# Optimization experiments

Measured on AMD Instinct MI355X. Metric: run time of the kernel, lower is better.

The kernel has to match this reference:

```python
import jax, jax.numpy as jnp
import numpy as np

NB_STEPS = 50
ALPHA = 0.9
NUM_RNN_STEPS = 2
B = 4096
NUM_FEATURE = 100
IN_D = 5
HIDDEN = [64, 64, 64]
P1 = (1.1, 1.1, 1.5, 2.0, 2.5)   # IntegrandNN_outer_level powers
P2 = (1.5, 2.0, 2.5, 3.0, 3.5)   # IntegrandNN powers


def _cc(nb_steps):
    # Clenshaw-Curtis weights/steps, identical to UMNN's compute_cc_weights
    n = nb_steps
    i = np.arange(n + 1, dtype=np.float64).reshape(-1, 1)
    lam = np.cos(i @ i.T * np.pi / n)
    lam[:, 0] = 0.5
    lam[:, -1] *= 0.5
    lam = lam * 2.0 / n
    W = np.zeros(n + 1)
    even = np.arange(0, n + 1, 2)
    W[even] = 2.0 / (1.0 - even.astype(np.float64) ** 2)
    W[0] = 1.0
    ccw = (lam.T @ W).astype(np.float32)                         # [n+1]
    steps = np.cos(np.arange(n + 1) * np.pi / n).astype(np.float32)  # [n+1]
    return jnp.asarray(ccw), jnp.asarray(steps)

CC_W, CC_S = _cc(NB_STEPS)


def _mlp(xh, Ws, bs):
    # Linear+ReLU stack with ELU on the last layer (ReLU popped, ELU appended)
    h = xh
    for W, b in zip(Ws[:-1], bs[:-1]):
        h = jax.nn.relu(h @ W.T + b)
    return jax.nn.elu(h @ Ws[-1].T + bs[-1])


def _integrand(x, h, Ws, bs, Wf, powers):
    z = _mlp(jnp.concatenate([x, h], axis=1), Ws, bs) + 1.0      # [N,1], z >= 0
    feats = jnp.concatenate([z ** p for p in powers], axis=1)    # [N,5]
    return jax.nn.relu((1.0 / (feats + 1.0)) @ Wf.T)             # [N,1]


def _integrate(x0, xT, h, f):
    # ParallelNeuralIntegral forward: CC quadrature of f from x0 to xT
    Bn, S = x0.shape[0], NB_STEPS + 1
    X = x0[:, None, :] + (xT - x0)[:, None, :] * (CC_S[None, :, None] + 1.0) / 2.0  # [B,S,1]
    hs = jnp.broadcast_to(h[:, None, :], (Bn, S, h.shape[1])).reshape(-1, h.shape[1])
    dz = f(X.reshape(-1, 1), hs).reshape(Bn, S, 1)
    return (dz * CC_W[None, :, None]).sum(1) * (xT - x0) / 2.0   # [B,1]


def setup_inputs() -> dict:
    key = jax.random.key(0)
    ks = jax.random.split(key, 24)
    def lin(k, o, i):
        return jax.random.normal(k, (o, i), jnp.float32) / np.sqrt(i)
    d = {}
    d["x_"] = jax.random.normal(ks[0], (B, NUM_FEATURE), jnp.float32)
    d["h_"] = jax.random.normal(ks[1], (B, IN_D - 1), jnp.float32)
    d["log_weight"] = jnp.ones((1, NUM_FEATURE), jnp.float32)     # reset_parameters -> 1
    d["sigmoid_param"] = jnp.zeros((1,), jnp.float32)
    sizes = [IN_D] + HIDDEN + [1]
    for tag, base in (("f1", 2), ("f2", 12)):
        for li, (i, o) in enumerate(zip(sizes[:-1], sizes[1:])):
            d[f"{tag}_W{li}"] = lin(ks[base + 2 * li], o, i)
            d[f"{tag}_b{li}"] = jnp.zeros((o,), jnp.float32)
        d[f"{tag}_Wf"] = jnp.abs(lin(ks[base + 9], 1, 5))         # reset_params -> abs
    return d


def reference(x_, h_, log_weight, sigmoid_param,
              f1_W0, f1_b0, f1_W1, f1_b1, f1_W2, f1_b2, f1_W3, f1_b3, f1_Wf,
              f2_W0, f2_b0, f2_W1, f2_b1, f2_W2, f2_b2, f2_W3, f2_b3, f2_Wf):
    f1Ws = [f1_W0, f1_W1, f1_W2, f1_W3]; f1bs = [f1_b0, f1_b1, f1_b2, f1_b3]
    f2Ws = [f2_W0, f2_W1, f2_W2, f2_W3]; f2bs = [f2_b0, f2_b1, f2_b2, f2_b3]
    f1 = lambda x, h: _integrand(x, h, f1Ws, f1bs, f1_Wf, P1)
    f2 = lambda x, h: _integrand(x, h, f2Ws, f2bs, f2_Wf, P2)

    # modular function: linear to [B,1] then sum over dim 1 -> [B,1]
    xm = jnp.sum(x_ * log_weight[0], axis=1, keepdims=True)
    lam = jax.nn.sigmoid(sigmoid_param[0])

    I1 = jnp.zeros_like(xm)
    I2 = jnp.zeros_like(xm)
    out_first = None
    for _ in range(NUM_RNN_STEPS):
        x = (1.0 - lam) * xm + lam * I1
        x2 = (1.0 - lam) * xm + lam * I2
        out_first = f1(x2, h_)
        I1 = _integrate(jnp.zeros_like(x), x, h_, f1)
        xmax = jnp.max(x2) + 10.0
        xfinal = jnp.zeros_like(x) + xmax
        I2 = (1.0 / ALPHA) * _integrate(x2, xfinal, h_, f2)
    return I1, out_first, I2
```

## Files before the change

### kernel.cpp

```cpp
#include <hip/hip_runtime.h>
#include <math.h>

typedef _Float16 half8v __attribute__((ext_vector_type(8)));
typedef _Float16 half4v __attribute__((ext_vector_type(4)));
typedef _Float16 half2v __attribute__((ext_vector_type(2)));
typedef float float4v __attribute__((ext_vector_type(4)));

#define BB    4096
#define NS    51
#define INV_ALPHA (1.0f/0.9f)

#define WS_CCW   0
#define WS_CCS   64
#define WS_LAM   128
#define WS_KEY64 160
#define WS_PM    256
#define WS_XM    512
#define WS_X     (WS_XM + BB)
#define WS_X2    (WS_X + BB)
#define WS_H     16384
#define H_NET    8192
#define H_W2     4096
#define H_W0     16384
#define H_W3     20480

#if defined(__has_builtin)
#if __has_builtin(__builtin_amdgcn_rcpf)
#define FRCP(x) __builtin_amdgcn_rcpf(x)
#endif
#if __has_builtin(__builtin_amdgcn_exp2f)
#define FEXP2(x) __builtin_amdgcn_exp2f(x)
#endif
#if __has_builtin(__builtin_amdgcn_logf)
#define FLOG2(x) __builtin_amdgcn_logf(x)
#endif
#endif
#ifndef FRCP
#define FRCP(x) (1.0f / (x))
#endif
#ifndef FEXP2
#define FEXP2(x) exp2f(x)
#endif
#ifndef FLOG2
#define FLOG2(x) log2f(x)
#endif

__device__ __forceinline__ unsigned fkey(float f) {
    int i = __float_as_int(f);
    return (i >= 0) ? ((unsigned)i + 0x80000000u) : ~(unsigned)i;
}
__device__ __forceinline__ float fkey_inv(unsigned k) {
    return (k & 0x80000000u) ? __int_as_float((int)(k - 0x80000000u))
                             : __int_as_float((int)~k);
}

__device__ __forceinline__ int swz(int row, int cb) {
    return (row << 6) + (((cb ^ (row & 7)) & 7) << 3);
}

__device__ __forceinline__ half4v pk_relu4(float4v c) {
#if defined(__has_builtin) && __has_builtin(__builtin_amdgcn_cvt_pkrtz)
    half2v a = __builtin_bit_cast(half2v,
        __builtin_amdgcn_cvt_pkrtz(fmaxf(c[0], 0.0f), fmaxf(c[1], 0.0f)));
    half2v b = __builtin_bit_cast(half2v,
        __builtin_amdgcn_cvt_pkrtz(fmaxf(c[2], 0.0f), fmaxf(c[3], 0.0f)));
    half4v o; o[0] = a[0]; o[1] = a[1]; o[2] = b[0]; o[3] = b[1];
    return o;
#else
    half4v o;
    o[0] = (_Float16)fmaxf(c[0], 0.0f); o[1] = (_Float16)fmaxf(c[1], 0.0f);
    o[2] = (_Float16)fmaxf(c[2], 0.0f); o[3] = (_Float16)fmaxf(c[3], 0.0f);
    return o;
#endif
}

__global__ void k_setup(const float* __restrict__ x_, const float* __restrict__ lw,
                        const float* __restrict__ sp,
                        const float* __restrict__ f1W0, const float* __restrict__ f1W1,
                        const float* __restrict__ f1W2, const float* __restrict__ f1W3,
                        const float* __restrict__ f2W0, const float* __restrict__ f2W1,
                        const float* __restrict__ f2W2, const float* __restrict__ f2W3,
                        float* __restrict__ ws) {
    _Float16* wh = (_Float16*)(ws + WS_H);
    const int blk = blockIdx.x, tid = threadIdx.x;
    if (blk < 256) {
        int wave = tid >> 6, lane = tid & 63;
        float vmax = -1e30f;
        for (int r = 0; r < 4; ++r) {
            int row = blk * 16 + wave * 4 + r;
            float v = 0.0f;
            for (int i = lane; i < 100; i += 64) v = fmaf(x_[row * 100 + i], lw[i], v);
            #pragma unroll
            for (int off = 32; off > 0; off >>= 1) v += __shfl_xor(v, off, 64);
            if (lane == 0) ws[WS_XM + row] = v;
            vmax = fmaxf(vmax, v);
        }
        __shared__ float sm[4];
        if (lane == 0) sm[wave] = vmax;
        __syncthreads();
        if (tid == 0)
            ws[WS_PM + blk] = fmaxf(fmaxf(sm[0], sm[1]), fmaxf(sm[2], sm[3]));
    } else if (blk < 272) {
        int t = (blk - 256) * 256 + tid;
        wh[t]                = (_Float16)f1W1[t];
        wh[H_W2 + t]         = (_Float16)f1W2[t];
        wh[H_NET + t]        = (_Float16)f2W1[t];
        wh[H_NET + H_W2 + t] = (_Float16)f2W2[t];
        if (t < 2048) {
            int j = t >> 5, k = t & 31;
            wh[H_W0 + t]        = (k < 5) ? (_Float16)f1W0[j * 5 + k] : (_Float16)0.0f;
            wh[H_W0 + 2048 + t] = (k < 5) ? (_Float16)f2W0[j * 5 + k] : (_Float16)0.0f;
        }
        if (t < 64) {
            wh[H_W3 + t]      = (_Float16)f1W3[t];
            wh[H_W3 + 64 + t] = (_Float16)f2W3[t];
        }
    } else {
        if (tid < 64) ((unsigned*)ws)[WS_KEY64 + tid] = 0u;
        if (tid == 64) ws[WS_LAM] = 1.0f / (1.0f + expf(-sp[0]));
        if (tid >= 128 && tid <= 178) {
            int s = tid - 128;
            ws[WS_CCS + s] = cospif((float)s / 50.0f);
            float acc = 0.0f;
            for (int a = 0; a <= 50; ++a) {
                float w;
                if (a == 0) w = 1.0f;
                else if ((a & 1) == 0) w = 2.0f / (1.0f - (float)(a * a));
                else continue;
                float l;
                if (s == 0) l = 0.5f;
                else {
                    int m = (a * s) % 100;
                    l = cospif((float)m / 50.0f);
                    if (s == 50) l *= 0.5f;
                }
                acc += l * 0.04f * w;
            }
            ws[WS_CCW + s] = acc;
        }
    }
}

__global__ __launch_bounds__(64, 4) void k_int(
    int mode, float* __restrict__ ws, const float* __restrict__ h_,
    const float* __restrict__ f1b0, const float* __restrict__ f1b1,
    const float* __restrict__ f1b2, const float* __restrict__ f1b3,
    const float* __restrict__ f1Wf,
    const float* __restrict__ f2b0, const float* __restrict__ f2b1,
    const float* __restrict__ f2b2, const float* __restrict__ f2b3,
    const float* __restrict__ f2Wf,
    float* __restrict__ out)
{
    __shared__ _Float16 act[64 * 64];

    const int blk = blockIdx.x;
    const int lane = threadIdx.x;
    const int lo = lane & 15, q = lane >> 4;

    const float* xm = ws + WS_XM;
    const float* xarr = ws + WS_X;
    const float* x2arr = ws + WS_X2;
    const _Float16* wh = (const _Float16*)(ws + WS_H);
    const float lam = ws[WS_LAM];
    const float oml = 1.0f - lam;

    int kind, b = 0, b0 = 0;
    if (blk < 4096)      { kind = 0; b = blk; }
    else if (blk < 8192) { kind = 1; b = blk - 4096; }
    else                 { kind = 2; b0 = (blk - 8192) * 64; b = b0 + lane; }

    float xmax = 0.0f, xb = 0.0f, x0 = 0.0f;
    float4 h4u = {0, 0, 0, 0};
    if (kind == 0) {
        xb = mode ? xarr[b] : oml * xm[b];
        h4u = ((const float4*)h_)[b];
    } else if (kind == 1) {
        if (mode) {
            float v = fkey_inv(((const unsigned*)ws)[WS_KEY64 + lane]);
            #pragma unroll
            for (int off = 32; off > 0; off >>= 1) v = fmaxf(v, __shfl_xor(v, off, 64));
            xmax = v + 10.0f;
        } else {
            const float* pm = ws + WS_PM;
            float v = fmaxf(fmaxf(pm[lane], pm[lane + 64]),
                            fmaxf(pm[lane + 128], pm[lane + 192]));
            #pragma unroll
            for (int off = 32; off > 0; off >>= 1) v = fmaxf(v, __shfl_xor(v, off, 64));
            xmax = oml * v + 10.0f;
        }
        x0 = mode ? x2arr[b] : oml * xm[b];
        h4u = ((const float4*)h_)[b];
    }

    const bool u2 = (kind == 1);
    const _Float16* W0h = wh + H_W0 + (u2 ? 2048 : 0);
    const _Float16* W1h = wh + (u2 ? H_NET : 0);
    const _Float16* W2h = W1h + H_W2;
    const _Float16* W3h = wh + H_W3 + (u2 ? 64 : 0);
    const float* B0 = u2 ? f2b0 : f1b0;
    const float* B1 = u2 ? f2b1 : f1b1;
    const float* B2 = u2 ? f2b2 : f1b2;
    const float* B3 = u2 ? f2b3 : f1b3;
    const float* WF = u2 ? f2Wf : f1Wf;
    const float p0 = u2 ? 1.5f : 1.1f;
    const float p1 = u2 ? 2.0f : 1.1f;
    const float p2 = u2 ? 2.5f : 1.5f;
    const float p3 = u2 ? 3.0f : 2.0f;
    const float p4 = u2 ? 3.5f : 2.5f;

    {
        half8v Bf0[4];
        #pragma unroll
        for (int n = 0; n < 4; ++n) {
            int r = 16 * n + lo;
            float xr; float4 hr;
            if (kind == 2) {
                int idx = b0 + r;
                xr = x2arr[idx];
                hr = ((const float4*)h_)[idx];
            } else {
                int si = r > 50 ? 50 : r;
                float t = (ws[WS_CCS + si] + 1.0f) * 0.5f;
                xr = (kind == 0) ? xb * t : x0 + (xmax - x0) * t;
                hr = h4u;
            }
            half8v e;
            e[0] = (_Float16)xr; e[1] = (_Float16)hr.x; e[2] = (_Float16)hr.y;
            e[3] = (_Float16)hr.z; e[4] = (_Float16)hr.w;
            e[5] = (_Float16)0.0f; e[6] = (_Float16)0.0f; e[7] = (_Float16)0.0f;
            half8v z;
            #pragma unroll
            for (int t2 = 0; t2 < 8; ++t2) z[t2] = (_Float16)0.0f;
            Bf0[n] = (q == 0) ? e : z;
        }
        #pragma unroll
        for (int m = 0; m < 4; ++m) {
            half8v Af = *(const half8v*)(W0h + (16 * m + lo) * 32 + q * 8);
            float4v bb = *(const float4v*)(B0 + 16 * m + q * 4);
            #pragma unroll
            for (int n = 0; n < 4; ++n) {
                float4v c = __builtin_amdgcn_mfma_f32_16x16x32_f16(Af, Bf0[n], bb, 0, 0, 0);
                *(half4v*)(act + swz(16 * n + lo, 2 * m + (q >> 1)) + 4 * (q & 1)) = pk_relu4(c);
            }
        }
    }

    {
        half8v Bf[2][4];
        #pragma unroll
        for (int kb = 0; kb < 2; ++kb)
            #pragma unroll
            for (int n = 0; n < 4; ++n)
                Bf[kb][n] = *(const half8v*)(act + swz(16 * n + lo, 4 * kb + q));
        #pragma unroll
        for (int m = 0; m < 4; ++m) {
            half8v A0 = *(const half8v*)(W1h + (16 * m + lo) * 64 + q * 8);
            half8v A1 = *(const half8v*)(W1h + (16 * m + lo) * 64 + 32 + q * 8);
            float4v bb = *(const float4v*)(B1 + 16 * m + q * 4);
            #pragma unroll
            for (int n = 0; n < 4; ++n) {
                float4v c = __builtin_amdgcn_mfma_f32_16x16x32_f16(A0, Bf[0][n], bb, 0, 0, 0);
                c = __builtin_amdgcn_mfma_f32_16x16x32_f16(A1, Bf[1][n], c, 0, 0, 0);
                *(half4v*)(act + swz(16 * n + lo, 2 * m + (q >> 1)) + 4 * (q & 1)) = pk_relu4(c);
            }
        }
    }

    float part[4] = {0.0f, 0.0f, 0.0f, 0.0f};
    {
        half8v Bf[2][4];
        #pragma unroll
        for (int kb = 0; kb < 2; ++kb)
            #pragma unroll
            for (int n = 0; n < 4; ++n)
                Bf[kb][n] = *(const half8v*)(act + swz(16 * n + lo, 4 * kb + q));
        #pragma unroll
        for (int m = 0; m < 4; ++m) {
            half8v A0 = *(const half8v*)(W2h + (16 * m + lo) * 64 + q * 8);
            half8v A1 = *(const half8v*)(W2h + (16 * m + lo) * 64 + 32 + q * 8);
            float4v bb = *(const float4v*)(B2 + 16 * m + q * 4);
            half4v w3 = *(const half4v*)(W3h + 16 * m + 4 * q);
            #pragma unroll
            for (int n = 0; n < 4; ++n) {
                float4v c = __builtin_amdgcn_mfma_f32_16x16x32_f16(A0, Bf[0][n], bb, 0, 0, 0);
                c = __builtin_amdgcn_mfma_f32_16x16x32_f16(A1, Bf[1][n], c, 0, 0, 0);
                #pragma unroll
                for (int e = 0; e < 4; ++e)
                    part[n] = fmaf((float)w3[e], fmaxf(c[e], 0.0f), part[n]);
            }
        }
    }

    #pragma unroll
    for (int n = 0; n < 4; ++n) {
        part[n] += __shfl_xor(part[n], 16, 64);
        part[n] += __shfl_xor(part[n], 32, 64);
    }
    float y = B3[0] + (q == 0 ? part[0] : q == 1 ? part[1] : q == 2 ? part[2] : part[3]);

    if (y <= 0.0f) y = FEXP2(y * 1.44269504f) - 1.0f;
    float z = y + 1.0f;
    float lg = FLOG2(z);
    float g = WF[0] * FRCP(FEXP2(p0 * lg) + 1.0f)
            + WF[1] * FRCP(FEXP2(p1 * lg) + 1.0f)
            + WF[2] * FRCP(FEXP2(p2 * lg) + 1.0f)
            + WF[3] * FRCP(FEXP2(p3 * lg) + 1.0f)
            + WF[4] * FRCP(FEXP2(p4 * lg) + 1.0f);
    float val = fmaxf(g, 0.0f);

    if (kind == 2) { out[BB + b] = val; return; }

    float c = (lane <= 50) ? ws[WS_CCW + lane] * val : 0.0f;
    #pragma unroll
    for (int off = 32; off > 0; off >>= 1) c += __shfl_xor(c, off, 64);

    if (lane == 0) {
        if (kind == 0) {
            float I1 = c * xb * 0.5f;
            out[b] = I1;
            if (!mode) ws[WS_X + b] = oml * xm[b] + lam * I1;
        } else {
            float I2 = c * (xmax - x0) * 0.5f * INV_ALPHA;
            out[2 * BB + b] = I2;
            if (!mode) {
                float x2n = oml * xm[b] + lam * I2;
                ws[WS_X2 + b] = x2n;
                atomicMax((unsigned*)ws + WS_KEY64 + (b & 63), fkey(x2n));
            }
        }
    }
}

extern "C" void kernel_launch(void* const* d_in, const int* in_sizes, int n_in,
                              void* d_out, int out_size, void* d_ws, size_t ws_size,
                              hipStream_t stream) {
    const float* x_  = (const float*)d_in[0];
    const float* h_  = (const float*)d_in[1];
    const float* lw  = (const float*)d_in[2];
    const float* sp  = (const float*)d_in[3];
    const float* f1W0 = (const float*)d_in[4];   const float* f1b0 = (const float*)d_in[5];
    const float* f1W1 = (const float*)d_in[6];   const float* f1b1 = (const float*)d_in[7];
    const float* f1W2 = (const float*)d_in[8];   const float* f1b2 = (const float*)d_in[9];
    const float* f1W3 = (const float*)d_in[10];  const float* f1b3 = (const float*)d_in[11];
    const float* f1Wf = (const float*)d_in[12];
    const float* f2W0 = (const float*)d_in[13];  const float* f2b0 = (const float*)d_in[14];
    const float* f2W1 = (const float*)d_in[15];  const float* f2b1 = (const float*)d_in[16];
    const float* f2W2 = (const float*)d_in[17];  const float* f2b2 = (const float*)d_in[18];
    const float* f2W3 = (const float*)d_in[19];  const float* f2b3 = (const float*)d_in[20];
    const float* f2Wf = (const float*)d_in[21];
    float* out = (float*)d_out;
    float* ws  = (float*)d_ws;

    k_setup<<<273, 256, 0, stream>>>(x_, lw, sp,
                                     f1W0, f1W1, f1W2, f1W3,
                                     f2W0, f2W1, f2W2, f2W3, ws);
    k_int<<<8192, 64, 0, stream>>>(0, ws, h_,
        f1b0, f1b1, f1b2, f1b3, f1Wf, f2b0, f2b1, f2b2, f2b3, f2Wf, out);
    k_int<<<8256, 64, 0, stream>>>(1, ws, h_,
        f1b0, f1b1, f1b2, f1b3, f1Wf, f2b0, f2b1, f2b2, f2b3, f2Wf, out);
}
```

Baseline: 158.2 us.

## Make integrand kernel persistent and keep MLP weights in registers across items

The integration kernel now launches 2048 blocks, and each loops over four batch items (plus one out_first tile for 64 blocks in mode 1). The weights, biases, quadrature steps and weights are loaded into registers once per block instead of once per item. Launch bounds drop from 4 to 2 waves per EU to make room for the extra registers. This cuts repeated weight loads and block launch overhead, but lowers occupancy and leaves the out_first tiles as a tail on 64 blocks.

Result: faster. 144.9 us (-8.4%).

```diff
diff --git a/kernel.cpp b/kernel.cpp
--- a/kernel.cpp
+++ b/kernel.cpp
@@ -141,7 +141,7 @@
     }
 }
 
-__global__ __launch_bounds__(64, 4) void k_int(
+__global__ __launch_bounds__(64, 2) void k_int(
     int mode, float* __restrict__ ws, const float* __restrict__ h_,
     const float* __restrict__ f1b0, const float* __restrict__ f1b1,
     const float* __restrict__ f1b2, const float* __restrict__ f1b3,
@@ -164,35 +164,9 @@
     const float lam = ws[WS_LAM];
     const float oml = 1.0f - lam;
 
-    int kind, b = 0, b0 = 0;
-    if (blk < 4096)      { kind = 0; b = blk; }
-    else if (blk < 8192) { kind = 1; b = blk - 4096; }
-    else                 { kind = 2; b0 = (blk - 8192) * 64; b = b0 + lane; }
-
-    float xmax = 0.0f, xb = 0.0f, x0 = 0.0f;
-    float4 h4u = {0, 0, 0, 0};
-    if (kind == 0) {
-        xb = mode ? xarr[b] : oml * xm[b];
-        h4u = ((const float4*)h_)[b];
-    } else if (kind == 1) {
-        if (mode) {
-            float v = fkey_inv(((const unsigned*)ws)[WS_KEY64 + lane]);
-            #pragma unroll
-            for (int off = 32; off > 0; off >>= 1) v = fmaxf(v, __shfl_xor(v, off, 64));
-            xmax = v + 10.0f;
-        } else {
-            const float* pm = ws + WS_PM;
-            float v = fmaxf(fmaxf(pm[lane], pm[lane + 64]),
-                            fmaxf(pm[lane + 128], pm[lane + 192]));
-            #pragma unroll
-            for (int off = 32; off > 0; off >>= 1) v = fmaxf(v, __shfl_xor(v, off, 64));
-            xmax = oml * v + 10.0f;
-        }
-        x0 = mode ? x2arr[b] : oml * xm[b];
-        h4u = ((const float4*)h_)[b];
-    }
-
-    const bool u2 = (kind == 1);
+    const bool u2 = (blk >= 1024);
+    const int kb0 = u2 ? blk - 1024 : blk;
+
     const _Float16* W0h = wh + H_W0 + (u2 ? 2048 : 0);
     const _Float16* W1h = wh + (u2 ? H_NET : 0);
     const _Float16* W2h = W1h + H_W2;
@@ -208,124 +182,177 @@
     const float p3 = u2 ? 3.0f : 2.0f;
     const float p4 = u2 ? 3.5f : 2.5f;
 
-    {
+    half8v A0w[4], A1w[4][2], A2w[4][2];
+    float4v b0r[4], b1r[4], b2r[4];
+    half4v w3r[4];
+    #pragma unroll
+    for (int m = 0; m < 4; ++m) {
+        A0w[m]    = *(const half8v*)(W0h + (16 * m + lo) * 32 + q * 8);
+        A1w[m][0] = *(const half8v*)(W1h + (16 * m + lo) * 64 + q * 8);
+        A1w[m][1] = *(const half8v*)(W1h + (16 * m + lo) * 64 + 32 + q * 8);
+        A2w[m][0] = *(const half8v*)(W2h + (16 * m + lo) * 64 + q * 8);
+        A2w[m][1] = *(const half8v*)(W2h + (16 * m + lo) * 64 + 32 + q * 8);
+        b0r[m] = *(const float4v*)(B0 + 16 * m + q * 4);
+        b1r[m] = *(const float4v*)(B1 + 16 * m + q * 4);
+        b2r[m] = *(const float4v*)(B2 + 16 * m + q * 4);
+        w3r[m] = *(const half4v*)(W3h + 16 * m + 4 * q);
+    }
+    const float B3s = B3[0];
+    const float wf0 = WF[0], wf1 = WF[1], wf2 = WF[2], wf3 = WF[3], wf4 = WF[4];
+
+    float t_r[4];
+    #pragma unroll
+    for (int n = 0; n < 4; ++n) {
+        int r = 16 * n + lo;
+        t_r[n] = (ws[WS_CCS + (r > 50 ? 50 : r)] + 1.0f) * 0.5f;
+    }
+    const float ccw_l = (lane <= 50) ? ws[WS_CCW + lane] : 0.0f;
+
+    float xmax = 0.0f;
+    if (u2) {
+        if (mode) {
+            float v = fkey_inv(((const unsigned*)ws)[WS_KEY64 + lane]);
+            #pragma unroll
+            for (int off = 32; off > 0; off >>= 1) v = fmaxf(v, __shfl_xor(v, off, 64));
+            xmax = v + 10.0f;
+        } else {
+            const float* pm = ws + WS_PM;
+            float v = fmaxf(fmaxf(pm[lane], pm[lane + 64]),
+                            fmaxf(pm[lane + 128], pm[lane + 192]));
+            #pragma unroll
+            for (int off = 32; off > 0; off >>= 1) v = fmaxf(v, __shfl_xor(v, off, 64));
+            xmax = oml * v + 10.0f;
+        }
+    }
+
+    const int nitems = (mode && !u2 && blk < 64) ? 5 : 4;
+
+    #pragma clang loop unroll(disable)
+    for (int it = 0; it < nitems; ++it) {
+        const bool last = (it == 4);
+        int b = kb0 + 1024 * it;
+        float xb = 0.0f, x0 = 0.0f;
+        float4 h4u = {0, 0, 0, 0};
+
         half8v Bf0[4];
+        if (last) {
+            int b0i = blk * 64;
+            #pragma unroll
+            for (int n = 0; n < 4; ++n) {
+                int idx = b0i + 16 * n + lo;
+                float xr = x2arr[idx];
+                float4 hr = ((const float4*)h_)[idx];
+                half8v e;
+                e[0] = (_Float16)xr; e[1] = (_Float16)hr.x; e[2] = (_Float16)hr.y;
+                e[3] = (_Float16)hr.z; e[4] = (_Float16)hr.w;
+                e[5] = (_Float16)0.0f; e[6] = (_Float16)0.0f; e[7] = (_Float16)0.0f;
+                half8v z;
+                #pragma unroll
+                for (int t2 = 0; t2 < 8; ++t2) z[t2] = (_Float16)0.0f;
+                Bf0[n] = (q == 0) ? e : z;
+            }
+        } else {
+            if (!u2) xb = mode ? xarr[b] : oml * xm[b];
+            else     x0 = mode ? x2arr[b] : oml * xm[b];
+            h4u = ((const float4*)h_)[b];
+            #pragma unroll
+            for (int n = 0; n < 4; ++n) {
+                float xr = (!u2) ? xb * t_r[n] : x0 + (xmax - x0) * t_r[n];
+                half8v e;
+                e[0] = (_Float16)xr; e[1] = (_Float16)h4u.x; e[2] = (_Float16)h4u.y;
+                e[3] = (_Float16)h4u.z; e[4] = (_Float16)h4u.w;
+                e[5] = (_Float16)0.0f; e[6] = (_Float16)0.0f; e[7] = (_Float16)0.0f;
+                half8v z;
+                #pragma unroll
+                for (int t2 = 0; t2 < 8; ++t2) z[t2] = (_Float16)0.0f;
+                Bf0[n] = (q == 0) ? e : z;
+            }
+        }
+
+        #pragma unroll
+        for (int m = 0; m < 4; ++m)
+            #pragma unroll
+            for (int n = 0; n < 4; ++n) {
+                float4v c = __builtin_amdgcn_mfma_f32_16x16x32_f16(A0w[m], Bf0[n], b0r[m], 0, 0, 0);
+                *(half4v*)(act + swz(16 * n + lo, 2 * m + (q >> 1)) + 4 * (q & 1)) = pk_relu4(c);
+            }
+
+        {
+            half8v Bf[2][4];
+            #pragma unroll
+            for (int kb = 0; kb < 2; ++kb)
+                #pragma unroll
+                for (int n = 0; n < 4; ++n)
+                    Bf[kb][n] = *(const half8v*)(act + swz(16 * n + lo, 4 * kb + q));
+            #pragma unroll
+            for (int m = 0; m < 4; ++m)
+                #pragma unroll
+                for (int n = 0; n < 4; ++n) {
+                    float4v c = __builtin_amdgcn_mfma_f32_16x16x32_f16(A1w[m][0], Bf[0][n], b1r[m], 0, 0, 0);
+                    c = __builtin_amdgcn_mfma_f32_16x16x32_f16(A1w[m][1], Bf[1][n], c, 0, 0, 0);
+                    *(half4v*)(act + swz(16 * n + lo, 2 * m + (q >> 1)) + 4 * (q & 1)) = pk_relu4(c);
+                }
+        }
+
+        float part[4] = {0.0f, 0.0f, 0.0f, 0.0f};
+        {
+            half8v Bf[2][4];
+            #pragma unroll
+            for (int kb = 0; kb < 2; ++kb)
+                #pragma unroll
+                for (int n = 0; n < 4; ++n)
+                    Bf[kb][n] = *(const half8v*)(act + swz(16 * n + lo, 4 * kb + q));
+            #pragma unroll
+            for (int m = 0; m < 4; ++m)
+                #pragma unroll
+                for (int n = 0; n < 4; ++n) {
+                    float4v c = __builtin_amdgcn_mfma_f32_16x16x32_f16(A2w[m][0], Bf[0][n], b2r[m], 0, 0, 0);
+                    c = __builtin_amdgcn_mfma_f32_16x16x32_f16(A2w[m][1], Bf[1][n], c, 0, 0, 0);
+                    #pragma unroll
+                    for (int e = 0; e < 4; ++e)
+                        part[n] = fmaf((float)w3r[m][e], fmaxf(c[e], 0.0f), part[n]);
+                }
+        }
+
         #pragma unroll
         for (int n = 0; n < 4; ++n) {
-            int r = 16 * n + lo;
-            float xr; float4 hr;
-            if (kind == 2) {
-                int idx = b0 + r;
-                xr = x2arr[idx];
-                hr = ((const float4*)h_)[idx];
+            part[n] += __shfl_xor(part[n], 16, 64);
+            part[n] += __shfl_xor(part[n], 32, 64);
+        }
+        float y = B3s + (q == 0 ? part[0] : q == 1 ? part[1] : q == 2 ? part[2] : part[3]);
+
+        if (y <= 0.0f) y = FEXP2(y * 1.44269504f) - 1.0f;
+        float z = y + 1.0f;
+        float lg = FLOG2(z);
+        float g = wf0 * FRCP(FEXP2(p0 * lg) + 1.0f)
+                + wf1 * FRCP(FEXP2(p1 * lg) + 1.0f)
+                + wf2 * FRCP(FEXP2(p2 * lg) + 1.0f)
+                + wf3 * FRCP(FEXP2(p3 * lg) + 1.0f)
+                + wf4 * FRCP(FEXP2(p4 * lg) + 1.0f);
+        float val = fmaxf(g, 0.0f);
+
+        if (last) {
+            out[BB + blk * 64 + lane] = val;
+            continue;
+        }
+
+        float c = ccw_l * val;
+        #pragma unroll
+        for (int off = 32; off > 0; off >>= 1) c += __shfl_xor(c, off, 64);
+
+        if (lane == 0) {
+            if (!u2) {
+                float I1 = c * xb * 0.5f;
+                out[b] = I1;
+                if (!mode) ws[WS_X + b] = oml * xm[b] + lam * I1;
             } else {
-                int si = r > 50 ? 50 : r;
-                float t = (ws[WS_CCS + si] + 1.0f) * 0.5f;
-                xr = (kind == 0) ? xb * t : x0 + (xmax - x0) * t;
-                hr = h4u;
-            }
-            half8v e;
-            e[0] = (_Float16)xr; e[1] = (_Float16)hr.x; e[2] = (_Float16)hr.y;
-            e[3] = (_Float16)hr.z; e[4] = (_Float16)hr.w;
-            e[5] = (_Float16)0.0f; e[6] = (_Float16)0.0f; e[7] = (_Float16)0.0f;
-            half8v z;
-            #pragma unroll
-            for (int t2 = 0; t2 < 8; ++t2) z[t2] = (_Float16)0.0f;
-            Bf0[n] = (q == 0) ? e : z;
-        }
-        #pragma unroll
-        for (int m = 0; m < 4; ++m) {
-            half8v Af = *(const half8v*)(W0h + (16 * m + lo) * 32 + q * 8);
-            float4v bb = *(const float4v*)(B0 + 16 * m + q * 4);
-            #pragma unroll
-            for (int n = 0; n < 4; ++n) {
-                float4v c = __builtin_amdgcn_mfma_f32_16x16x32_f16(Af, Bf0[n], bb, 0, 0, 0);
-                *(half4v*)(act + swz(16 * n + lo, 2 * m + (q >> 1)) + 4 * (q & 1)) = pk_relu4(c);
-            }
-        }
-    }
-
-    {
-        half8v Bf[2][4];
-        #pragma unroll
-        for (int kb = 0; kb < 2; ++kb)
-            #pragma unroll
-            for (int n = 0; n < 4; ++n)
-                Bf[kb][n] = *(const half8v*)(act + swz(16 * n + lo, 4 * kb + q));
-        #pragma unroll
-        for (int m = 0; m < 4; ++m) {
-            half8v A0 = *(const half8v*)(W1h + (16 * m + lo) * 64 + q * 8);
-            half8v A1 = *(const half8v*)(W1h + (16 * m + lo) * 64 + 32 + q * 8);
-            float4v bb = *(const float4v*)(B1 + 16 * m + q * 4);
-            #pragma unroll
-            for (int n = 0; n < 4; ++n) {
-                float4v c = __builtin_amdgcn_mfma_f32_16x16x32_f16(A0, Bf[0][n], bb, 0, 0, 0);
-                c = __builtin_amdgcn_mfma_f32_16x16x32_f16(A1, Bf[1][n], c, 0, 0, 0);
-                *(half4v*)(act + swz(16 * n + lo, 2 * m + (q >> 1)) + 4 * (q & 1)) = pk_relu4(c);
-            }
-        }
-    }
-
-    float part[4] = {0.0f, 0.0f, 0.0f, 0.0f};
-    {
-        half8v Bf[2][4];
-        #pragma unroll
-        for (int kb = 0; kb < 2; ++kb)
-            #pragma unroll
-            for (int n = 0; n < 4; ++n)
-                Bf[kb][n] = *(const half8v*)(act + swz(16 * n + lo, 4 * kb + q));
-        #pragma unroll
-        for (int m = 0; m < 4; ++m) {
-            half8v A0 = *(const half8v*)(W2h + (16 * m + lo) * 64 + q * 8);
-            half8v A1 = *(const half8v*)(W2h + (16 * m + lo) * 64 + 32 + q * 8);
-            float4v bb = *(const float4v*)(B2 + 16 * m + q * 4);
-            half4v w3 = *(const half4v*)(W3h + 16 * m + 4 * q);
-            #pragma unroll
-            for (int n = 0; n < 4; ++n) {
-                float4v c = __builtin_amdgcn_mfma_f32_16x16x32_f16(A0, Bf[0][n], bb, 0, 0, 0);
-                c = __builtin_amdgcn_mfma_f32_16x16x32_f16(A1, Bf[1][n], c, 0, 0, 0);
-                #pragma unroll
-                for (int e = 0; e < 4; ++e)
-                    part[n] = fmaf((float)w3[e], fmaxf(c[e], 0.0f), part[n]);
-            }
-        }
-    }
-
-    #pragma unroll
-    for (int n = 0; n < 4; ++n) {
-        part[n] += __shfl_xor(part[n], 16, 64);
-        part[n] += __shfl_xor(part[n], 32, 64);
-    }
-    float y = B3[0] + (q == 0 ? part[0] : q == 1 ? part[1] : q == 2 ? part[2] : part[3]);
-
-    if (y <= 0.0f) y = FEXP2(y * 1.44269504f) - 1.0f;
-    float z = y + 1.0f;
-    float lg = FLOG2(z);
-    float g = WF[0] * FRCP(FEXP2(p0 * lg) + 1.0f)
-            + WF[1] * FRCP(FEXP2(p1 * lg) + 1.0f)
-            + WF[2] * FRCP(FEXP2(p2 * lg) + 1.0f)
-            + WF[3] * FRCP(FEXP2(p3 * lg) + 1.0f)
-            + WF[4] * FRCP(FEXP2(p4 * lg) + 1.0f);
-    float val = fmaxf(g, 0.0f);
-
-    if (kind == 2) { out[BB + b] = val; return; }
-
-    float c = (lane <= 50) ? ws[WS_CCW + lane] * val : 0.0f;
-    #pragma unroll
-    for (int off = 32; off > 0; off >>= 1) c += __shfl_xor(c, off, 64);
-
-    if (lane == 0) {
-        if (kind == 0) {
-            float I1 = c * xb * 0.5f;
-            out[b] = I1;
-            if (!mode) ws[WS_X + b] = oml * xm[b] + lam * I1;
-        } else {
-            float I2 = c * (xmax - x0) * 0.5f * INV_ALPHA;
-            out[2 * BB + b] = I2;
-            if (!mode) {
-                float x2n = oml * xm[b] + lam * I2;
-                ws[WS_X2 + b] = x2n;
-                atomicMax((unsigned*)ws + WS_KEY64 + (b & 63), fkey(x2n));
+                float I2 = c * (xmax - x0) * 0.5f * INV_ALPHA;
+                out[2 * BB + b] = I2;
+                if (!mode) {
+                    float x2n = oml * xm[b] + lam * I2;
+                    ws[WS_X2 + b] = x2n;
+                    atomicMax((unsigned*)ws + WS_KEY64 + (b & 63), fkey(x2n));
+                }
             }
         }
     }
@@ -354,8 +381,8 @@
     k_setup<<<273, 256, 0, stream>>>(x_, lw, sp,
                                      f1W0, f1W1, f1W2, f1W3,
                                      f2W0, f2W1, f2W2, f2W3, ws);
-    k_int<<<8192, 64, 0, stream>>>(0, ws, h_,
+    k_int<<<2048, 64, 0, stream>>>(0, ws, h_,
         f1b0, f1b1, f1b2, f1b3, f1Wf, f2b0, f2b1, f2b2, f2b3, f2Wf, out);
-    k_int<<<8256, 64, 0, stream>>>(1, ws, h_,
+    k_int<<<2048, 64, 0, stream>>>(1, ws, h_,
         f1b0, f1b1, f1b2, f1b3, f1Wf, f2b0, f2b1, f2b2, f2b3, f2Wf, out);
 }
```
